# Performance work log

Measured on AMD Instinct MI355X. Metric: run time of the kernel, lower is better.

Reference implementation:

```python
import jax, jax.numpy as jnp
import numpy as np

MARGIN = 1.0
N = 8192
NUM_PROPS = 32

def setup_inputs() -> dict:
    key = jax.random.key(0)
    k1, k2, k3 = jax.random.split(key, 3)
    scores = jax.random.normal(k1, (N,), dtype=jnp.float32)
    labels = jax.random.randint(k2, (N,), 0, 2, dtype=jnp.int32)
    property_ids = jax.random.randint(k3, (N,), 0, NUM_PROPS, dtype=jnp.int32)
    return {"scores": scores, "labels": labels, "property_ids": property_ids}

def reference(scores, labels, property_ids):
    s = scores.reshape(-1)
    lab = labels.reshape(-1)
    pid = property_ids.reshape(-1)
    # pair (i, j) is valid iff same property, label_i == 1, label_j == 0
    mask = (pid[:, None] == pid[None, :]) & (lab == 1)[:, None] & (lab == 0)[None, :]  # [N, N] bool
    diffs = s[:, None] - s[None, :]  # [N, N]
    per_pair = jnp.where(mask, jnp.maximum(MARGIN - diffs, 0.0), 0.0)
    total_loss = per_pair.sum()
    num_pairs = mask.sum()
    # reduction='mean' over valid pairs; 0.0 if no valid pairs
    return jnp.where(num_pairs == 0, jnp.float32(0.0), total_loss / num_pairs.astype(s.dtype))
```

## Files before the change

### kernel.cpp

```cpp
#include <hip/hip_runtime.h>

#define NPROPS 32
#define MAXN   8192
#define MARGIN 1.0f

struct Ws {
    double    loss[NPROPS];
    long long pairs[NPROPS];
};

__global__ __launch_bounds__(256)
void fused_kernel(const float* __restrict__ scores,
                  const int*   __restrict__ labels,
                  const int*   __restrict__ pids,
                  Ws* __restrict__ ws, int n) {
    const int p   = blockIdx.x;
    const int tid = threadIdx.x;

    __shared__ float pos_s[MAXN];
    __shared__ float neg_s[MAXN];
    __shared__ int   cnt[2];

    if (tid < 2) cnt[tid] = 0;
    __syncthreads();

    const int4*   pid4v = (const int4*)pids;
    const int4*   lab4v = (const int4*)labels;
    const float4* sc4v  = (const float4*)scores;
    for (int v = tid; v * 4 < n; v += 256) {
        int4   pd = pid4v[v];
        int4   lb = lab4v[v];
        float4 sc = sc4v[v];
        #pragma unroll
        for (int k = 0; k < 4; ++k) {
            int   pk = (&pd.x)[k];
            int   lk = (&lb.x)[k];
            float sk = (&sc.x)[k];
            if (pk == p) {
                int idx = atomicAdd(&cnt[lk], 1);
                if (lk) pos_s[idx] = sk; else neg_s[idx] = sk;
            }
        }
    }
    __syncthreads();

    const int nneg = cnt[0];
    const int npos = cnt[1];

    float acc = 0.0f;
    for (int i = tid; i < npos; i += 256) {
        const float a = MARGIN - pos_s[i];
        for (int j = 0; j < nneg; ++j)
            acc += fmaxf(a + neg_s[j], 0.0f);
    }

    #pragma unroll
    for (int off = 32; off > 0; off >>= 1)
        acc += __shfl_down(acc, off);

    __shared__ float wsum[4];
    const int lane = tid & 63, wid = tid >> 6;
    if (lane == 0) wsum[wid] = acc;
    __syncthreads();

    if (tid == 0) {
        ws->loss[p]  = (double)(wsum[0] + wsum[1] + wsum[2] + wsum[3]);
        ws->pairs[p] = (long long)npos * (long long)nneg;
    }
}

__global__ __launch_bounds__(64)
void finalize_kernel(const Ws* __restrict__ ws, float* __restrict__ out) {
    const int lane = threadIdx.x;
    double    l = (lane < NPROPS) ? ws->loss[lane]  : 0.0;
    long long c = (lane < NPROPS) ? ws->pairs[lane] : 0;
    #pragma unroll
    for (int off = 32; off > 0; off >>= 1) {
        l += __shfl_down(l, off);
        c += __shfl_down(c, off);
    }
    if (lane == 0) out[0] = (c == 0) ? 0.0f : (float)(l / (double)c);
}

extern "C" void kernel_launch(void* const* d_in, const int* in_sizes, int n_in,
                              void* d_out, int out_size, void* d_ws, size_t ws_size,
                              hipStream_t stream) {
    const float* scores = (const float*)d_in[0];
    const int*   labels = (const int*)d_in[1];
    const int*   pids   = (const int*)d_in[2];
    const int    n      = in_sizes[0];
    Ws* ws = (Ws*)d_ws;

    fused_kernel<<<NPROPS, 256, 0, stream>>>(scores, labels, pids, ws, n);
    finalize_kernel<<<1, 64, 0, stream>>>(ws, (float*)d_out);
}
```

Measured before the change: 13.55 us.

## Merge per-property blocks into one 1024-thread block with counting-sort bucketing

```diff
diff --git a/kernel.cpp b/kernel.cpp
--- a/kernel.cpp
+++ b/kernel.cpp
@@ -1,85 +1,120 @@
 #include <hip/hip_runtime.h>
 
-#define NPROPS 32
-#define MAXN   8192
-#define MARGIN 1.0f
+#define NPROPS   32
+#define MAXN     8192
+#define NTHREADS 1024
+#define MARGIN   1.0f
 
-struct Ws {
-    double    loss[NPROPS];
-    long long pairs[NPROPS];
-};
+__global__ __launch_bounds__(NTHREADS)
+void fused1_kernel(const float* __restrict__ scores,
+                   const int*   __restrict__ labels,
+                   const int*   __restrict__ pids,
+                   float* __restrict__ out, int n) {
+    __shared__ float     neg_s[MAXN];
+    __shared__ float     pos_s[MAXN];
+    __shared__ int       pos_pid[MAXN];
+    __shared__ int       cnt[64];
+    __shared__ int       nbase[NPROPS + 1];
+    __shared__ int       pbase[NPROPS + 1];
+    __shared__ long long npairs;
+    __shared__ float     wsum[NTHREADS / 64];
 
-__global__ __launch_bounds__(256)
-void fused_kernel(const float* __restrict__ scores,
-                  const int*   __restrict__ labels,
-                  const int*   __restrict__ pids,
-                  Ws* __restrict__ ws, int n) {
-    const int p   = blockIdx.x;
-    const int tid = threadIdx.x;
+    const int tid  = threadIdx.x;
+    const int nvec = n >> 2;
 
-    __shared__ float pos_s[MAXN];
-    __shared__ float neg_s[MAXN];
-    __shared__ int   cnt[2];
+    int4   pd[2];
+    int4   lb[2];
+    float4 sc[2];
+    #pragma unroll
+    for (int it = 0; it < 2; ++it) {
+        const int v = tid + it * NTHREADS;
+        if (v < nvec) {
+            pd[it] = ((const int4*)pids)[v];
+            lb[it] = ((const int4*)labels)[v];
+            sc[it] = ((const float4*)scores)[v];
+        }
+    }
 
-    if (tid < 2) cnt[tid] = 0;
+    if (tid < 64) cnt[tid] = 0;
     __syncthreads();
 
-    const int4*   pid4v = (const int4*)pids;
-    const int4*   lab4v = (const int4*)labels;
-    const float4* sc4v  = (const float4*)scores;
-    for (int v = tid; v * 4 < n; v += 256) {
-        int4   pd = pid4v[v];
-        int4   lb = lab4v[v];
-        float4 sc = sc4v[v];
-        #pragma unroll
-        for (int k = 0; k < 4; ++k) {
-            int   pk = (&pd.x)[k];
-            int   lk = (&lb.x)[k];
-            float sk = (&sc.x)[k];
-            if (pk == p) {
-                int idx = atomicAdd(&cnt[lk], 1);
-                if (lk) pos_s[idx] = sk; else neg_s[idx] = sk;
+    #pragma unroll
+    for (int it = 0; it < 2; ++it) {
+        const int v = tid + it * NTHREADS;
+        if (v < nvec) {
+            #pragma unroll
+            for (int k = 0; k < 4; ++k) {
+                const int b = (&pd[it].x)[k] + ((&lb[it].x)[k] << 5);
+                atomicAdd(&cnt[b], 1);
             }
         }
     }
     __syncthreads();
 
-    const int nneg = cnt[0];
-    const int npos = cnt[1];
+    if (tid == 0) {
+        int o = 0;
+        for (int p = 0; p < NPROPS; ++p) { nbase[p] = o; o += cnt[p]; }
+        nbase[NPROPS] = o;
+        int o2 = 0;
+        long long pairs = 0;
+        for (int p = 0; p < NPROPS; ++p) {
+            pbase[p] = o2;
+            o2    += cnt[32 + p];
+            pairs += (long long)cnt[32 + p] * (long long)cnt[p];
+        }
+        pbase[NPROPS] = o2;
+        npairs = pairs;
+    }
+    __syncthreads();
 
+    if (tid < 32)                 cnt[tid] = nbase[tid];
+    else if (tid < 64)            cnt[tid] = pbase[tid - 32];
+    __syncthreads();
+
+    #pragma unroll
+    for (int it = 0; it < 2; ++it) {
+        const int v = tid + it * NTHREADS;
+        if (v < nvec) {
+            #pragma unroll
+            for (int k = 0; k < 4; ++k) {
+                const int   p   = (&pd[it].x)[k];
+                const int   lab = (&lb[it].x)[k];
+                const float s   = (&sc[it].x)[k];
+                if (lab) {
+                    const int idx = atomicAdd(&cnt[32 + p], 1);
+                    pos_s[idx]   = s;
+                    pos_pid[idx] = p;
+                } else {
+                    const int idx = atomicAdd(&cnt[p], 1);
+                    neg_s[idx] = s;
+                }
+            }
+        }
+    }
+    __syncthreads();
+
+    const int total_pos = pbase[NPROPS];
     float acc = 0.0f;
-    for (int i = tid; i < npos; i += 256) {
-        const float a = MARGIN - pos_s[i];
-        for (int j = 0; j < nneg; ++j)
+    for (int i = tid; i < total_pos; i += NTHREADS) {
+        const float a  = MARGIN - pos_s[i];
+        const int   p  = pos_pid[i];
+        const int   j1 = nbase[p + 1];
+        for (int j = nbase[p]; j < j1; ++j)
             acc += fmaxf(a + neg_s[j], 0.0f);
     }
 
     #pragma unroll
     for (int off = 32; off > 0; off >>= 1)
         acc += __shfl_down(acc, off);
-
-    __shared__ float wsum[4];
-    const int lane = tid & 63, wid = tid >> 6;
-    if (lane == 0) wsum[wid] = acc;
+    if ((tid & 63) == 0) wsum[tid >> 6] = acc;
     __syncthreads();
 
     if (tid == 0) {
-        ws->loss[p]  = (double)(wsum[0] + wsum[1] + wsum[2] + wsum[3]);
-        ws->pairs[p] = (long long)npos * (long long)nneg;
+        double t = 0.0;
+        #pragma unroll
+        for (int w = 0; w < NTHREADS / 64; ++w) t += (double)wsum[w];
+        out[0] = (npairs == 0) ? 0.0f : (float)(t / (double)npairs);
     }
-}
-
-__global__ __launch_bounds__(64)
-void finalize_kernel(const Ws* __restrict__ ws, float* __restrict__ out) {
-    const int lane = threadIdx.x;
-    double    l = (lane < NPROPS) ? ws->loss[lane]  : 0.0;
-    long long c = (lane < NPROPS) ? ws->pairs[lane] : 0;
-    #pragma unroll
-    for (int off = 32; off > 0; off >>= 1) {
-        l += __shfl_down(l, off);
-        c += __shfl_down(c, off);
-    }
-    if (lane == 0) out[0] = (c == 0) ? 0.0f : (float)(l / (double)c);
 }
 
 extern "C" void kernel_launch(void* const* d_in, const int* in_sizes, int n_in,
@@ -89,8 +124,7 @@
     const int*   labels = (const int*)d_in[1];
     const int*   pids   = (const int*)d_in[2];
     const int    n      = in_sizes[0];
-    Ws* ws = (Ws*)d_ws;
 
-    fused_kernel<<<NPROPS, 256, 0, stream>>>(scores, labels, pids, ws, n);
-    finalize_kernel<<<1, 64, 0, stream>>>(ws, (float*)d_out);
+    fused1_kernel<<<1, NTHREADS, 0, stream>>>(scores, labels, pids,
+                                              (float*)d_out, n);
 }
```

Result: slower. 38.58 us (+184.7%).

## Widen per-property block to 1024 threads and split pair loop across 8 lanes

Applied to the files above, without the earlier changes.

```diff
diff --git a/kernel.cpp b/kernel.cpp
--- a/kernel.cpp
+++ b/kernel.cpp
@@ -1,15 +1,16 @@
 #include <hip/hip_runtime.h>
 
-#define NPROPS 32
-#define MAXN   8192
-#define MARGIN 1.0f
+#define NPROPS   32
+#define BUCKCAP  1024
+#define NTHREADS 1024
+#define MARGIN   1.0f
 
 struct Ws {
     double    loss[NPROPS];
     long long pairs[NPROPS];
 };
 
-__global__ __launch_bounds__(256)
+__global__ __launch_bounds__(NTHREADS)
 void fused_kernel(const float* __restrict__ scores,
                   const int*   __restrict__ labels,
                   const int*   __restrict__ pids,
@@ -17,9 +18,10 @@
     const int p   = blockIdx.x;
     const int tid = threadIdx.x;
 
-    __shared__ float pos_s[MAXN];
-    __shared__ float neg_s[MAXN];
+    __shared__ float pos_s[BUCKCAP];
+    __shared__ float neg_s[BUCKCAP];
     __shared__ int   cnt[2];
+    __shared__ float wsum[NTHREADS / 64];
 
     if (tid < 2) cnt[tid] = 0;
     __syncthreads();
@@ -27,17 +29,17 @@
     const int4*   pid4v = (const int4*)pids;
     const int4*   lab4v = (const int4*)labels;
     const float4* sc4v  = (const float4*)scores;
-    for (int v = tid; v * 4 < n; v += 256) {
+    const int nvec = n >> 2;
+    for (int v = tid; v < nvec; v += NTHREADS) {
         int4   pd = pid4v[v];
         int4   lb = lab4v[v];
         float4 sc = sc4v[v];
         #pragma unroll
         for (int k = 0; k < 4; ++k) {
-            int   pk = (&pd.x)[k];
-            int   lk = (&lb.x)[k];
-            float sk = (&sc.x)[k];
-            if (pk == p) {
-                int idx = atomicAdd(&cnt[lk], 1);
+            if ((&pd.x)[k] == p) {
+                const int   lk  = (&lb.x)[k];
+                const int   idx = atomicAdd(&cnt[lk], 1);
+                const float sk  = (&sc.x)[k];
                 if (lk) pos_s[idx] = sk; else neg_s[idx] = sk;
             }
         }
@@ -48,23 +50,24 @@
     const int npos = cnt[1];
 
     float acc = 0.0f;
-    for (int i = tid; i < npos; i += 256) {
+    const int j0 = tid & 7;
+    for (int i = tid >> 3; i < npos; i += NTHREADS / 8) {
         const float a = MARGIN - pos_s[i];
-        for (int j = 0; j < nneg; ++j)
+        for (int j = j0; j < nneg; j += 8)
             acc += fmaxf(a + neg_s[j], 0.0f);
     }
 
     #pragma unroll
     for (int off = 32; off > 0; off >>= 1)
         acc += __shfl_down(acc, off);
-
-    __shared__ float wsum[4];
-    const int lane = tid & 63, wid = tid >> 6;
-    if (lane == 0) wsum[wid] = acc;
+    if ((tid & 63) == 0) wsum[tid >> 6] = acc;
     __syncthreads();
 
     if (tid == 0) {
-        ws->loss[p]  = (double)(wsum[0] + wsum[1] + wsum[2] + wsum[3]);
+        float s = 0.0f;
+        #pragma unroll
+        for (int w = 0; w < NTHREADS / 64; ++w) s += wsum[w];
+        ws->loss[p]  = (double)s;
         ws->pairs[p] = (long long)npos * (long long)nneg;
     }
 }
@@ -91,6 +94,6 @@
     const int    n      = in_sizes[0];
     Ws* ws = (Ws*)d_ws;
 
-    fused_kernel<<<NPROPS, 256, 0, stream>>>(scores, labels, pids, ws, n);
+    fused_kernel<<<NPROPS, NTHREADS, 0, stream>>>(scores, labels, pids, ws, n);
     finalize_kernel<<<1, 64, 0, stream>>>(ws, (float*)d_out);
 }
```

Result: faster. 11.73 us, median of 2 (-13.4%).
